# Kernel optimization log

Measured on AMD Instinct MI355X. Metric: run time of the kernel, lower is better.

The kernel has to match this reference:

```python
import jax, jax.numpy as jnp
import numpy as np

# Directional rectangle cumulative max: max over the axis-aligned rectangle
# between each pixel and one image corner.

def _rectmax(x, rev_h, rev_w):
    y = jax.lax.cummax(x, axis=2, reverse=rev_h)
    return jax.lax.cummax(y, axis=3, reverse=rev_w)


def _guided_pool(xq, gq, rev_h, rev_w):
    # Guided landmark pool: each pixel takes max of itself and the directional
    # cumulative max restricted to guide==1 positions. With guide == ones this
    # reduces to the plain directional rectangle cummax (the un-guided pool).
    neg = jnp.finfo(xq.dtype).min
    masked = jnp.where(gq > 0, xq, neg)
    return jnp.maximum(xq, _rectmax(masked, rev_h, rev_w))

# (rev_h, rev_w) for TopLeft, TopRight, BottomLeft, BottomRight pools
_DIRS = [(True, True), (True, False), (False, True), (False, False)]


def setup_inputs() -> dict:
    key = jax.random.key(0)
    k1, k2, k3 = jax.random.split(key, 3)
    B, C, H, W = 16, 256, 64, 64
    Cout, K = 256, 3
    x = jax.random.normal(k1, (B, C, H, W), jnp.float32)
    weight = jax.random.normal(k2, (Cout, C, K, K), jnp.float32) * 0.02
    bias = jax.random.normal(k3, (Cout,), jnp.float32) * 0.02
    return {"x": x, "weight": weight, "bias": bias}


def reference(x, weight, bias):
    B, C, H, W = x.shape
    Q = C // 4
    # Original torch code squares x IN PLACE via chunk() views before pooling.
    xsq = x * x
    # Per-quadrant channel energy and its global (row, col) argmax -> one-hot guide.
    energy = xsq.reshape(B, 4, Q, H, W).sum(axis=2)            # [B,4,H,W]
    idx = jnp.argmax(energy.reshape(B, 4, H * W), axis=-1)     # [B,4]
    onehot = (jnp.arange(H * W) == idx[..., None]).astype(x.dtype)
    guide = jnp.broadcast_to(onehot.reshape(B, 4, 1, H, W), (B, 4, Q, H, W)).reshape(B, C, H, W)
    # Four directional guided pools, one per channel quadrant, then conv.
    xs = jnp.split(xsq, 4, axis=1)
    gs = jnp.split(guide, 4, axis=1)
    pooled = jnp.concatenate(
        [_guided_pool(xs[i], gs[i], *_DIRS[i]) for i in range(4)], axis=1)
    out = jax.lax.conv_general_dilated(
        pooled, weight, window_strides=(1, 1), padding='SAME',
        dimension_numbers=('NCHW', 'OIHW', 'NCHW'))
    return out + bias[None, :, None, None]
```

## Files before the change

kernel.cpp:

```cpp
#include <hip/hip_runtime.h>
#include <cstddef>

#define B_   16
#define C_   256
#define HW_  4096

typedef __attribute__((ext_vector_type(8)))  short bf16x8;
typedef __attribute__((ext_vector_type(16))) float f32x16;

static __device__ __forceinline__ unsigned short f2bf(float f) {
    unsigned int u = __float_as_uint(f);
    u += 0x7fffu + ((u >> 16) & 1u);
    return (unsigned short)(u >> 16);
}

__global__ __launch_bounds__(256) void fused_energy(const float* __restrict__ x,
                                                    unsigned short* __restrict__ xsqN,
                                                    float* __restrict__ pval,
                                                    int* __restrict__ pidx) {
    int blk = blockIdx.x;
    int b = blk >> 6, h = blk & 63;
    int tid = threadIdx.x;
    int tl  = tid >> 4;
    int w4  = (tid & 15) << 2;
    int wv  = tid >> 6;
    __shared__ float earr[4][4][64];
    __shared__ unsigned short tile[64][264];
    const float* xb = x + (size_t)b * C_ * HW_ + h * 64 + w4;

    float e[4][4];
#pragma unroll
    for (int q = 0; q < 4; ++q)
#pragma unroll
        for (int ww = 0; ww < 4; ++ww) e[q][ww] = 0.f;

#pragma unroll
    for (int i = 0; i < 4; ++i) {
        int c4 = tl * 4 + 64 * i;
        float sq[4][4];
#pragma unroll
        for (int k = 0; k < 4; ++k) {
            float4 v = *(const float4*)(xb + (size_t)(c4 + k) * HW_);
            sq[k][0] = v.x * v.x; sq[k][1] = v.y * v.y;
            sq[k][2] = v.z * v.z; sq[k][3] = v.w * v.w;
            e[i][0] += sq[k][0]; e[i][1] += sq[k][1];
            e[i][2] += sq[k][2]; e[i][3] += sq[k][3];
        }
#pragma unroll
        for (int ww = 0; ww < 4; ++ww) {
            uint2 p;
            p.x = (unsigned)f2bf(sq[0][ww]) | ((unsigned)f2bf(sq[1][ww]) << 16);
            p.y = (unsigned)f2bf(sq[2][ww]) | ((unsigned)f2bf(sq[3][ww]) << 16);
            *(uint2*)(&tile[w4 + ww][c4]) = p;
        }
    }

#pragma unroll
    for (int q = 0; q < 4; ++q)
#pragma unroll
        for (int ww = 0; ww < 4; ++ww) {
            float v = e[q][ww];
            v += __shfl_xor(v, 16);
            v += __shfl_xor(v, 32);
            e[q][ww] = v;
        }
    if ((tid & 48) == 0) {
#pragma unroll
        for (int q = 0; q < 4; ++q) {
            float4 v; v.x = e[q][0]; v.y = e[q][1]; v.z = e[q][2]; v.w = e[q][3];
            *(float4*)&earr[wv][q][w4] = v;
        }
    }
    __syncthreads();

    size_t base = (size_t)(b * 64 + h) * 64 * 256;
#pragma unroll
    for (int it = 0; it < 8; ++it) {
        int row  = it * 8 + (tid >> 5);
        int col8 = (tid & 31) * 8;
        *(int4*)(xsqN + base + (size_t)row * 256 + col8) = *(int4*)&tile[row][col8];
    }

    int q = tid >> 6;
    int w = tid & 63;
    float ev = earr[0][q][w] + earr[1][q][w] + earr[2][q][w] + earr[3][q][w];
    int ix = h * 64 + w;
#pragma unroll
    for (int off = 32; off; off >>= 1) {
        float ov = __shfl_down(ev, off);
        int   oi = __shfl_down(ix, off);
        if (ov > ev || (ov == ev && oi < ix)) { ev = ov; ix = oi; }
    }
    if ((tid & 63) == 0) {
        pval[(b * 64 + h) * 4 + q] = ev;
        pidx[(b * 64 + h) * 4 + q] = ix;
    }
}

__global__ __launch_bounds__(64) void energy_final(const float* __restrict__ pval,
                                                   const int* __restrict__ pidx,
                                                   int* __restrict__ lm,
                                                   const unsigned short* __restrict__ xsqN,
                                                   unsigned short* __restrict__ Lval) {
    int bq = blockIdx.x;
    int b = bq >> 2, q = bq & 3;
    int t = threadIdx.x;
    float ev = pval[(b * 64 + t) * 4 + q];
    int   ix = pidx[(b * 64 + t) * 4 + q];
#pragma unroll
    for (int off = 32; off; off >>= 1) {
        float ov = __shfl_down(ev, off);
        int   oi = __shfl_down(ix, off);
        if (ov > ev || (ov == ev && oi < ix)) { ev = ov; ix = oi; }
    }
    int ix0 = __shfl(ix, 0);
    if (t == 0) lm[bq] = ix0;
    Lval[b * 256 + q * 64 + t] =
        xsqN[((size_t)((b * 64 + (ix0 >> 6)) * 64 + (ix0 & 63))) * 256 + q * 64 + t];
}

__global__ __launch_bounds__(256) void wt_pack(const float* __restrict__ w,
                                               unsigned short* __restrict__ wa) {
    int blk = blockIdx.x;
    int cog = blk >> 3, cib = blk & 7;
    int tid = threadIdx.x;
    __shared__ unsigned short wlds[32][292];
    {
        int co_l = tid >> 3;
        int seg  = tid & 7;
        const float* src = w + ((size_t)((cog * 32 + co_l) * 256 + cib * 32)) * 9 + seg * 36;
#pragma unroll
        for (int f4 = 0; f4 < 9; ++f4) {
            float4 v = *(const float4*)(src + f4 * 4);
            uint2 p;
            p.x = (unsigned)f2bf(v.x) | ((unsigned)f2bf(v.y) << 16);
            p.y = (unsigned)f2bf(v.z) | ((unsigned)f2bf(v.w) << 16);
            *(uint2*)(&wlds[co_l][seg * 36 + f4 * 4]) = p;
        }
    }
    __syncthreads();
    for (int idx = tid; idx < 1152; idx += 256) {
        int lane = idx & 63;
        int s    = (idx >> 6) & 1;
        int j    = idx >> 7;
        int co_l = lane & 31;
        int k0   = s * 16 + (lane >> 5) * 8;
        union { unsigned short us[8]; int4 v; } u;
#pragma unroll
        for (int jj = 0; jj < 8; ++jj)
            u.us[jj] = wlds[co_l][(k0 + jj) * 9 + j];
        int ob = (cib * 9 + j) * 16 + s * 8 + cog;
        *(int4*)(wa + ((size_t)ob * 64 + lane) * 8) = u.v;
    }
}

static __device__ __forceinline__ void load_B(int4 sv[4],
                                              const unsigned short* __restrict__ xsqN,
                                              int b, int h0, int nc, int tid) {
#pragma unroll
    for (int t2 = 0; t2 < 4; ++t2) {
        int idx = tid + t2 * 512;
        int4 v = {0, 0, 0, 0};
        if (idx < 1584) {
            int pr = idx / 264; int rem = idx - pr * 264;
            int pc = rem >> 2;  int part = rem & 3;
            int grow = h0 - 1 + pr, gcol = pc - 1;
            if ((unsigned)grow < 64u && (unsigned)gcol < 64u)
                v = *(const int4*)(xsqN + (((size_t)(b * 64 + grow) * 64 + gcol) * 256 + nc * 32 + part * 8));
        }
        sv[t2] = v;
    }
}

static __device__ __forceinline__ void store_B(const int4 sv[4],
                                               unsigned short* __restrict__ Bw,
                                               const unsigned short* __restrict__ Lval,
                                               const int* __restrict__ lm,
                                               int b, int h0, int nc, int tid) {
    int l = lm[b * 4 + (nc >> 1)];
    int hm = l >> 6, wm = l & 63;
    bool qhle = (nc >> 1) < 2;
    bool qwle = ((nc >> 1) & 1) == 0;
#pragma unroll
    for (int t2 = 0; t2 < 4; ++t2) {
        int idx = tid + t2 * 512;
        if (idx < 1584) {
            int pr = idx / 264; int rem = idx - pr * 264;
            int pc = rem >> 2;  int part = rem & 3;
            int grow = h0 - 1 + pr, gcol = pc - 1;
            union { int4 v; unsigned short us[8]; } u; u.v = sv[t2];
            bool inb = ((unsigned)grow < 64u) && ((unsigned)gcol < 64u);
            bool hok = qhle ? (grow <= hm) : (grow >= hm);
            bool wok = qwle ? (gcol <= wm) : (gcol >= wm);
            if (inb && hok && wok) {
                union { int4 v; unsigned short us[8]; } Lu;
                Lu.v = *(const int4*)(Lval + b * 256 + nc * 32 + part * 8);
#pragma unroll
                for (int k = 0; k < 8; ++k)
                    if (Lu.us[k] > u.us[k]) u.us[k] = Lu.us[k];
            }
            *(int4*)(&Bw[(pr * 66 + pc) * 40 + part * 8]) = u.v;
        }
    }
}

__global__ __launch_bounds__(512, 2) void conv_mfma(const unsigned short* __restrict__ xsqN,
                                                    const unsigned short* __restrict__ wa,
                                                    const float* __restrict__ bias,
                                                    const int* __restrict__ lm,
                                                    const unsigned short* __restrict__ Lval,
                                                    float* __restrict__ out) {
    int pt = blockIdx.x;
    int b  = pt >> 4;
    int h0 = (pt & 15) * 4;
    int tid  = threadIdx.x;
    int lane = tid & 63;
    int wv   = tid >> 6;
    int wy = wv >> 2, wx = wv & 3;
    int l31 = lane & 31, qh = lane >> 5;

    __shared__ unsigned short Bs[2][6 * 66 * 40];
    __shared__ unsigned short As[2][3 * 8192];

    f32x16 acc[4][2];
#pragma unroll
    for (int mt = 0; mt < 4; ++mt)
#pragma unroll
        for (int nt = 0; nt < 2; ++nt)
#pragma unroll
            for (int r = 0; r < 16; ++r) acc[mt][nt][r] = 0.f;

    {
        int4 sv[4];
        load_B(sv, xsqN, b, h0, 0, tid);
        const unsigned short* s0 = wa + wv * 3072 + lane * 8;
#pragma unroll
        for (int k = 0; k < 6; ++k)
            __builtin_amdgcn_global_load_lds(s0 + k * 512, &As[0][wv * 3072 + k * 512], 16, 0, 0);
        store_B(sv, &Bs[0][0], Lval, lm, b, h0, 0, tid);
    }
    __syncthreads();

    for (int cib = 0; cib < 8; ++cib) {
#pragma unroll
        for (int sub = 0; sub < 3; ++sub) {
            int ph = cib * 3 + sub;

            if (ph < 23) {
                const unsigned short* s0 = wa + (size_t)(ph + 1) * 24576 + wv * 3072 + lane * 8;
                unsigned short* d0 = &As[(ph + 1) & 1][wv * 3072];
#pragma unroll
                for (int k = 0; k < 6; ++k)
                    __builtin_amdgcn_global_load_lds(s0 + k * 512, d0 + k * 512, 16, 0, 0);
            }

            const unsigned short* Ab = &As[ph & 1][0];
            const unsigned short* Bb = &Bs[cib & 1][0];

            bf16x8 bf[2][2];
            bf16x8 aa[2][2];

            {
                const bf16x8* ap = (const bf16x8*)(Ab + (((wy * 4 + 0) * 64 + lane) << 3));
                aa[0][0] = ap[0];
                aa[0][1] = ap[512];
            }

#pragma unroll
            for (int tt = 0; tt < 3; ++tt) {
                int j  = sub * 3 + tt;
                int r  = wx + j / 3;
                int w0 = l31 + j % 3;
                const unsigned short* Bp = Bb + (r * 66 + w0) * 40 + qh * 8;
                bf[0][0] = *(const bf16x8*)(Bp);
                bf[0][1] = *(const bf16x8*)(Bp + 16);
                bf[1][0] = *(const bf16x8*)(Bp + 1280);
                bf[1][1] = *(const bf16x8*)(Bp + 1296);
#pragma unroll
                for (int m = 0; m < 4; ++m) {
                    const int p = m & 1;
                    if (m < 3) {
                        const bf16x8* ap = (const bf16x8*)(Ab + tt * 8192 + (((wy * 4 + m + 1) * 64 + lane) << 3));
                        aa[p ^ 1][0] = ap[0];
                        aa[p ^ 1][1] = ap[512];
                    } else if (tt < 2) {
                        const bf16x8* ap = (const bf16x8*)(Ab + (tt + 1) * 8192 + (((wy * 4 + 0) * 64 + lane) << 3));
                        aa[p ^ 1][0] = ap[0];
                        aa[p ^ 1][1] = ap[512];
                    }
                    acc[m][0] = __builtin_amdgcn_mfma_f32_32x32x16_bf16(aa[p][0], bf[0][0], acc[m][0], 0, 0, 0);
                    acc[m][1] = __builtin_amdgcn_mfma_f32_32x32x16_bf16(aa[p][0], bf[1][0], acc[m][1], 0, 0, 0);
                    acc[m][0] = __builtin_amdgcn_mfma_f32_32x32x16_bf16(aa[p][1], bf[0][1], acc[m][0], 0, 0, 0);
                    acc[m][1] = __builtin_amdgcn_mfma_f32_32x32x16_bf16(aa[p][1], bf[1][1], acc[m][1], 0, 0, 0);
                }
            }

            if (sub == 2 && cib < 7) {
                int4 sv[4];
                load_B(sv, xsqN, b, h0, cib + 1, tid);
                store_B(sv, &Bs[(cib + 1) & 1][0], Lval, lm, b, h0, cib + 1, tid);
            }

            __syncthreads();
        }
    }

    int h = h0 + wx;
#pragma unroll
    for (int mt = 0; mt < 4; ++mt) {
#pragma unroll
        for (int nt = 0; nt < 2; ++nt) {
#pragma unroll
            for (int r = 0; r < 16; ++r) {
                int row = (r & 3) + 8 * (r >> 2) + 4 * qh;
                int co  = wy * 128 + mt * 32 + row;
                int w   = nt * 32 + l31;
                out[(((size_t)(b * 256 + co)) * 64 + h) * 64 + w] = acc[mt][nt][r] + bias[co];
            }
        }
    }
}

extern "C" void kernel_launch(void* const* d_in, const int* in_sizes, int n_in,
                              void* d_out, int out_size, void* d_ws, size_t ws_size,
                              hipStream_t stream) {
    const float* x      = (const float*)d_in[0];
    const float* weight = (const float*)d_in[1];
    const float* bias   = (const float*)d_in[2];
    float* out = (float*)d_out;

    char* ws = (char*)d_ws;
    int*            lmp  = (int*)ws;
    float*          pval = (float*)(ws + 256);
    int*            pidx = (int*)(ws + 256 + 16384);
    unsigned short* Lval = (unsigned short*)(ws + 256 + 32768);
    unsigned short* Wa   = (unsigned short*)(ws + 49152);
    unsigned short* xsqN = (unsigned short*)(ws + 49152 + 1179648);

    hipLaunchKernelGGL(fused_energy, dim3(1024), dim3(256), 0, stream, x, xsqN, pval, pidx);
    hipLaunchKernelGGL(energy_final, dim3(64), dim3(64), 0, stream, pval, pidx, lmp, xsqN, Lval);
    hipLaunchKernelGGL(wt_pack, dim3(64), dim3(256), 0, stream, weight, Wa);
    hipLaunchKernelGGL(conv_mfma, dim3(256), dim3(512), 0, stream, xsqN, Wa, bias, lmp, Lval, out);
}
```

Baseline: 187.2 us.

## Merge weight packing into energy kernel and fold final argmax into conv

Weight packing is merged into the energy kernel by appending 64 extra blocks, with the two kernels' shared memory overlaid in a union. The final per-quadrant argmax reduction and the landmark value gather move into the conv kernel's prologue, where each block recomputes them into shared memory. Together these cut the launch sequence from four kernels to two, removing launch gaps and small serialized kernels. In exchange every conv block repeats the small reduction and adds two extra barriers before its first tile.

```diff
diff --git a/kernel.cpp b/kernel.cpp
--- a/kernel.cpp
+++ b/kernel.cpp
@@ -14,18 +14,57 @@
     return (unsigned short)(u >> 16);
 }
 
-__global__ __launch_bounds__(256) void fused_energy(const float* __restrict__ x,
-                                                    unsigned short* __restrict__ xsqN,
-                                                    float* __restrict__ pval,
-                                                    int* __restrict__ pidx) {
+__global__ __launch_bounds__(256) void fe_wp(const float* __restrict__ x,
+                                             unsigned short* __restrict__ xsqN,
+                                             float* __restrict__ pval,
+                                             int* __restrict__ pidx,
+                                             const float* __restrict__ w,
+                                             unsigned short* __restrict__ wa) {
+    __shared__ union {
+        struct { float earr[4][4][64]; unsigned short tile[64][264]; } fe;
+        unsigned short wlds[32][292];
+    } sm;
+
+    int tid = threadIdx.x;
+
+    if (blockIdx.x >= 1024) {
+        int blk = blockIdx.x - 1024;
+        int cog = blk >> 3, cib = blk & 7;
+        {
+            int co_l = tid >> 3;
+            int seg  = tid & 7;
+            const float* src = w + ((size_t)((cog * 32 + co_l) * 256 + cib * 32)) * 9 + seg * 36;
+#pragma unroll
+            for (int f4 = 0; f4 < 9; ++f4) {
+                float4 v = *(const float4*)(src + f4 * 4);
+                uint2 p;
+                p.x = (unsigned)f2bf(v.x) | ((unsigned)f2bf(v.y) << 16);
+                p.y = (unsigned)f2bf(v.z) | ((unsigned)f2bf(v.w) << 16);
+                *(uint2*)(&sm.wlds[co_l][seg * 36 + f4 * 4]) = p;
+            }
+        }
+        __syncthreads();
+        for (int idx = tid; idx < 1152; idx += 256) {
+            int lane = idx & 63;
+            int s    = (idx >> 6) & 1;
+            int j    = idx >> 7;
+            int co_l = lane & 31;
+            int k0   = s * 16 + (lane >> 5) * 8;
+            union { unsigned short us[8]; int4 v; } u;
+#pragma unroll
+            for (int jj = 0; jj < 8; ++jj)
+                u.us[jj] = sm.wlds[co_l][(k0 + jj) * 9 + j];
+            int ob = (cib * 9 + j) * 16 + s * 8 + cog;
+            *(int4*)(wa + ((size_t)ob * 64 + lane) * 8) = u.v;
+        }
+        return;
+    }
+
     int blk = blockIdx.x;
     int b = blk >> 6, h = blk & 63;
-    int tid = threadIdx.x;
     int tl  = tid >> 4;
     int w4  = (tid & 15) << 2;
     int wv  = tid >> 6;
-    __shared__ float earr[4][4][64];
-    __shared__ unsigned short tile[64][264];
     const float* xb = x + (size_t)b * C_ * HW_ + h * 64 + w4;
 
     float e[4][4];
@@ -51,7 +90,7 @@
             uint2 p;
             p.x = (unsigned)f2bf(sq[0][ww]) | ((unsigned)f2bf(sq[1][ww]) << 16);
             p.y = (unsigned)f2bf(sq[2][ww]) | ((unsigned)f2bf(sq[3][ww]) << 16);
-            *(uint2*)(&tile[w4 + ww][c4]) = p;
+            *(uint2*)(&sm.fe.tile[w4 + ww][c4]) = p;
         }
     }
 
@@ -68,7 +107,7 @@
 #pragma unroll
         for (int q = 0; q < 4; ++q) {
             float4 v; v.x = e[q][0]; v.y = e[q][1]; v.z = e[q][2]; v.w = e[q][3];
-            *(float4*)&earr[wv][q][w4] = v;
+            *(float4*)&sm.fe.earr[wv][q][w4] = v;
         }
     }
     __syncthreads();
@@ -78,13 +117,13 @@
     for (int it = 0; it < 8; ++it) {
         int row  = it * 8 + (tid >> 5);
         int col8 = (tid & 31) * 8;
-        *(int4*)(xsqN + base + (size_t)row * 256 + col8) = *(int4*)&tile[row][col8];
+        *(int4*)(xsqN + base + (size_t)row * 256 + col8) = *(int4*)&sm.fe.tile[row][col8];
     }
 
     int q = tid >> 6;
-    int w = tid & 63;
-    float ev = earr[0][q][w] + earr[1][q][w] + earr[2][q][w] + earr[3][q][w];
-    int ix = h * 64 + w;
+    int ww = tid & 63;
+    float ev = sm.fe.earr[0][q][ww] + sm.fe.earr[1][q][ww] + sm.fe.earr[2][q][ww] + sm.fe.earr[3][q][ww];
+    int ix = h * 64 + ww;
 #pragma unroll
     for (int off = 32; off; off >>= 1) {
         float ov = __shfl_down(ev, off);
@@ -94,63 +133,6 @@
     if ((tid & 63) == 0) {
         pval[(b * 64 + h) * 4 + q] = ev;
         pidx[(b * 64 + h) * 4 + q] = ix;
-    }
-}
-
-__global__ __launch_bounds__(64) void energy_final(const float* __restrict__ pval,
-                                                   const int* __restrict__ pidx,
-                                                   int* __restrict__ lm,
-                                                   const unsigned short* __restrict__ xsqN,
-                                                   unsigned short* __restrict__ Lval) {
-    int bq = blockIdx.x;
-    int b = bq >> 2, q = bq & 3;
-    int t = threadIdx.x;
-    float ev = pval[(b * 64 + t) * 4 + q];
-    int   ix = pidx[(b * 64 + t) * 4 + q];
-#pragma unroll
-    for (int off = 32; off; off >>= 1) {
-        float ov = __shfl_down(ev, off);
-        int   oi = __shfl_down(ix, off);
-        if (ov > ev || (ov == ev && oi < ix)) { ev = ov; ix = oi; }
-    }
-    int ix0 = __shfl(ix, 0);
-    if (t == 0) lm[bq] = ix0;
-    Lval[b * 256 + q * 64 + t] =
-        xsqN[((size_t)((b * 64 + (ix0 >> 6)) * 64 + (ix0 & 63))) * 256 + q * 64 + t];
-}
-
-__global__ __launch_bounds__(256) void wt_pack(const float* __restrict__ w,
-                                               unsigned short* __restrict__ wa) {
-    int blk = blockIdx.x;
-    int cog = blk >> 3, cib = blk & 7;
-    int tid = threadIdx.x;
-    __shared__ unsigned short wlds[32][292];
-    {
-        int co_l = tid >> 3;
-        int seg  = tid & 7;
-        const float* src = w + ((size_t)((cog * 32 + co_l) * 256 + cib * 32)) * 9 + seg * 36;
-#pragma unroll
-        for (int f4 = 0; f4 < 9; ++f4) {
-            float4 v = *(const float4*)(src + f4 * 4);
-            uint2 p;
-            p.x = (unsigned)f2bf(v.x) | ((unsigned)f2bf(v.y) << 16);
-            p.y = (unsigned)f2bf(v.z) | ((unsigned)f2bf(v.w) << 16);
-            *(uint2*)(&wlds[co_l][seg * 36 + f4 * 4]) = p;
-        }
-    }
-    __syncthreads();
-    for (int idx = tid; idx < 1152; idx += 256) {
-        int lane = idx & 63;
-        int s    = (idx >> 6) & 1;
-        int j    = idx >> 7;
-        int co_l = lane & 31;
-        int k0   = s * 16 + (lane >> 5) * 8;
-        union { unsigned short us[8]; int4 v; } u;
-#pragma unroll
-        for (int jj = 0; jj < 8; ++jj)
-            u.us[jj] = wlds[co_l][(k0 + jj) * 9 + j];
-        int ob = (cib * 9 + j) * 16 + s * 8 + cog;
-        *(int4*)(wa + ((size_t)ob * 64 + lane) * 8) = u.v;
     }
 }
 
@@ -174,10 +156,10 @@
 
 static __device__ __forceinline__ void store_B(const int4 sv[4],
                                                unsigned short* __restrict__ Bw,
-                                               const unsigned short* __restrict__ Lval,
-                                               const int* __restrict__ lm,
-                                               int b, int h0, int nc, int tid) {
-    int l = lm[b * 4 + (nc >> 1)];
+                                               const unsigned short* __restrict__ Lv,
+                                               const int* __restrict__ lmq,
+                                               int h0, int nc, int tid) {
+    int l = lmq[nc >> 1];
     int hm = l >> 6, wm = l & 63;
     bool qhle = (nc >> 1) < 2;
     bool qwle = ((nc >> 1) & 1) == 0;
@@ -194,7 +176,7 @@
             bool wok = qwle ? (gcol <= wm) : (gcol >= wm);
             if (inb && hok && wok) {
                 union { int4 v; unsigned short us[8]; } Lu;
-                Lu.v = *(const int4*)(Lval + b * 256 + nc * 32 + part * 8);
+                Lu.v = *(const int4*)(Lv + nc * 32 + part * 8);
 #pragma unroll
                 for (int k = 0; k < 8; ++k)
                     if (Lu.us[k] > u.us[k]) u.us[k] = Lu.us[k];
@@ -207,8 +189,8 @@
 __global__ __launch_bounds__(512, 2) void conv_mfma(const unsigned short* __restrict__ xsqN,
                                                     const unsigned short* __restrict__ wa,
                                                     const float* __restrict__ bias,
-                                                    const int* __restrict__ lm,
-                                                    const unsigned short* __restrict__ Lval,
+                                                    const float* __restrict__ pval,
+                                                    const int* __restrict__ pidx,
                                                     float* __restrict__ out) {
     int pt = blockIdx.x;
     int b  = pt >> 4;
@@ -221,6 +203,8 @@
 
     __shared__ unsigned short Bs[2][6 * 66 * 40];
     __shared__ unsigned short As[2][3 * 8192];
+    __shared__ __align__(16) unsigned short Lv[256];
+    __shared__ int lmq[4];
 
     f32x16 acc[4][2];
 #pragma unroll
@@ -231,13 +215,35 @@
             for (int r = 0; r < 16; ++r) acc[mt][nt][r] = 0.f;
 
     {
+        const unsigned short* s0 = wa + wv * 3072 + lane * 8;
+#pragma unroll
+        for (int k = 0; k < 6; ++k)
+            __builtin_amdgcn_global_load_lds(s0 + k * 512, &As[0][wv * 3072 + k * 512], 16, 0, 0);
+
         int4 sv[4];
         load_B(sv, xsqN, b, h0, 0, tid);
-        const unsigned short* s0 = wa + wv * 3072 + lane * 8;
-#pragma unroll
-        for (int k = 0; k < 6; ++k)
-            __builtin_amdgcn_global_load_lds(s0 + k * 512, &As[0][wv * 3072 + k * 512], 16, 0, 0);
-        store_B(sv, &Bs[0][0], Lval, lm, b, h0, 0, tid);
+
+        if (wv < 4) {
+            int q = wv;
+            float ev = pval[(b * 64 + lane) * 4 + q];
+            int   ix = pidx[(b * 64 + lane) * 4 + q];
+#pragma unroll
+            for (int off = 32; off; off >>= 1) {
+                float ov = __shfl_down(ev, off);
+                int   oi = __shfl_down(ix, off);
+                if (ov > ev || (ov == ev && oi < ix)) { ev = ov; ix = oi; }
+            }
+            if (lane == 0) lmq[q] = ix;
+        }
+        __syncthreads();
+        if (tid < 256) {
+            int c = tid, q = c >> 6;
+            int l = lmq[q];
+            Lv[c] = xsqN[((size_t)((b * 64 + (l >> 6)) * 64 + (l & 63))) * 256 + c];
+        }
+        __syncthreads();
+
+        store_B(sv, &Bs[0][0], Lv, lmq, h0, 0, tid);
     }
     __syncthreads();
 
@@ -298,7 +304,7 @@
             if (sub == 2 && cib < 7) {
                 int4 sv[4];
                 load_B(sv, xsqN, b, h0, cib + 1, tid);
-                store_B(sv, &Bs[(cib + 1) & 1][0], Lval, lm, b, h0, cib + 1, tid);
+                store_B(sv, &Bs[(cib + 1) & 1][0], Lv, lmq, h0, cib + 1, tid);
             }
 
             __syncthreads();
@@ -330,15 +336,11 @@
     float* out = (float*)d_out;
 
     char* ws = (char*)d_ws;
-    int*            lmp  = (int*)ws;
     float*          pval = (float*)(ws + 256);
     int*            pidx = (int*)(ws + 256 + 16384);
-    unsigned short* Lval = (unsigned short*)(ws + 256 + 32768);
     unsigned short* Wa   = (unsigned short*)(ws + 49152);
     unsigned short* xsqN = (unsigned short*)(ws + 49152 + 1179648);
 
-    hipLaunchKernelGGL(fused_energy, dim3(1024), dim3(256), 0, stream, x, xsqN, pval, pidx);
-    hipLaunchKernelGGL(energy_final, dim3(64), dim3(64), 0, stream, pval, pidx, lmp, xsqN, Lval);
-    hipLaunchKernelGGL(wt_pack, dim3(64), dim3(256), 0, stream, weight, Wa);
-    hipLaunchKernelGGL(conv_mfma, dim3(256), dim3(512), 0, stream, xsqN, Wa, bias, lmp, Lval, out);
-}
+    hipLaunchKernelGGL(fe_wp, dim3(1088), dim3(256), 0, stream, x, xsqN, pval, pidx, weight, Wa);
+    hipLaunchKernelGGL(conv_mfma, dim3(256), dim3(512), 0, stream, xsqN, Wa, bias, pval, pidx, out);
+}
```

Result: faster. 182.1 us (-2.8%).
